# Kernel tuning notes

Hardware: AMD Instinct MI355X
Metric: run time of the kernel (lower is better)

Reference implementation:

```python
import jax, jax.numpy as jnp
import numpy as np
import math

NUM_REG_TOKENS = 0  # encoder.num_register_tokens
EPS = 1e-12         # matches torch F.normalize eps


def _l2norm(x):
    # F.normalize(x, dim=-1): x / max(||x||, eps)
    n = jnp.sqrt(jnp.sum(x * x, axis=-1, keepdims=True))
    return x / jnp.maximum(n, EPS)


def setup_inputs() -> dict:
    key = jax.random.key(0)
    k1, k2 = jax.random.split(key)
    L, N, S, T, D = 3, 8, 4, 1370, 768  # 3 interested layers, T = 1 + 37^2 patches
    q_feats = jax.random.normal(k1, (L, N, T, D), dtype=jnp.float32)
    s_feats = jax.random.normal(k2, (L, N * S, T, D), dtype=jnp.float32)
    return {"q_feats": q_feats, "s_feats": s_feats}


def reference(q_feats, s_feats):
    # fuse_feature: mean over stacked interested layers
    xq = jnp.mean(q_feats, axis=0)   # [N, T, D]
    xs = jnp.mean(s_feats, axis=0)   # [N*S, T, D]
    N = xq.shape[0]
    Q = xq.shape[1] - 1 - NUM_REG_TOKENS
    side = int(math.isqrt(Q))
    # drop class (+register) tokens
    xq = xq[:, 1 + NUM_REG_TOKENS:, :]                 # [N, Q, D]
    xs = xs[:, 1 + NUM_REG_TOKENS:, :]                 # [N*S, Q, D]
    xs = xs.reshape(N, -1, xs.shape[-1])               # [N, S*Q, D]
    xq = _l2norm(xq)
    xs = _l2norm(xs)
    # cosine distance + 1-NN min over support tokens
    sim = jnp.einsum('nqd,nsd->nqs', xq, xs)           # [N, Q, S*Q]
    dist = jnp.min(1.0 - sim, axis=-1)                 # [N, Q]
    return dist.reshape(N, 1, side, side)
```

## Files before the change

### kernel.cpp

```cpp
#include <hip/hip_runtime.h>
#include <hip/hip_bf16.h>

typedef __attribute__((ext_vector_type(4))) float f32x4;

#define T_TOK 1370
#define DDIM  768
#define SCV   1369
#define SCP   1408
#define MQP   1536
#define NB    8
#define NSLAB 32
#define NST   44
#define NMT   6

#define MEMFENCE asm volatile("" ::: "memory")
#define BARRIER  do { __builtin_amdgcn_s_barrier(); MEMFENCE; } while (0)

#define GLOAD_LDS16(g, l)                                                     \
  __builtin_amdgcn_global_load_lds(                                           \
      (const __attribute__((address_space(1))) unsigned int*)(g),             \
      (__attribute__((address_space(3))) unsigned int*)(l), 16, 0, 0)

extern "C" __global__ __launch_bounds__(192) void prep_kernel(
    const float* __restrict__ src, unsigned char* __restrict__ dst,
    size_t lstride)
{
  const int row  = blockIdx.x;
  const int slab = blockIdx.y;
  const int t    = threadIdx.x;
  unsigned char* drow = dst + ((size_t)slab * gridDim.x + row) * DDIM;
  if (row >= SCV) {
    reinterpret_cast<unsigned int*>(drow)[t] = 0u;
    return;
  }
  const float* base = src + ((size_t)slab * T_TOK + row + 1) * DDIM;
  float4 a = reinterpret_cast<const float4*>(base)[t];
  float4 b = reinterpret_cast<const float4*>(base + lstride)[t];
  float4 c = reinterpret_cast<const float4*>(base + 2 * lstride)[t];
  const float k3 = 1.0f / 3.0f;
  float4 m;
  m.x = (a.x + b.x + c.x) * k3;
  m.y = (a.y + b.y + c.y) * k3;
  m.z = (a.z + b.z + c.z) * k3;
  m.w = (a.w + b.w + c.w) * k3;
  float ss = m.x * m.x + m.y * m.y + m.z * m.z + m.w * m.w;
  #pragma unroll
  for (int d = 1; d < 64; d <<= 1) ss += __shfl_xor(ss, d);
  __shared__ float wsum[3];
  if ((t & 63) == 0) wsum[t >> 6] = ss;
  __syncthreads();
  float tot = wsum[0] + wsum[1] + wsum[2];
  float rn = 1.0f / fmaxf(sqrtf(tot), 1e-12f);
  int pk = __builtin_amdgcn_cvt_pk_fp8_f32(m.x * rn, m.y * rn, 0, false);
  pk = __builtin_amdgcn_cvt_pk_fp8_f32(m.z * rn, m.w * rn, pk, true);
  reinterpret_cast<unsigned int*>(drow)[t] = (unsigned int)pk;
}

extern "C" __global__ __launch_bounds__(256, 2) void simmax_kernel(
    const unsigned char* __restrict__ xq,
    const unsigned char* __restrict__ xs,
    float* __restrict__ part)
{
  const int flat = blockIdx.x + NMT * (blockIdx.y + NST * blockIdx.z);
  const int swz  = (flat & 7) * (NMT * NST) + (flat >> 3);
  const int mt   = swz % NMT;
  const int st   = (swz / NMT) % NST;
  const int n    = swz / (NMT * NST);

  const int tid = threadIdx.x;
  const int lane = tid & 63;
  const int w    = tid >> 6;
  const int wr = w >> 1;
  const int wc = w & 1;
  const int l15 = lane & 15, l4 = lane >> 4;

  __shared__ unsigned char ring[3][12288];

  const int slab = st / 11;
  const int lt   = st - slab * 11;
  const unsigned char* gA = xq + ((size_t)n * MQP + (size_t)mt * 256) * DDIM;
  const unsigned char* gB =
      xs + ((size_t)(n * 4 + slab) * SCP + (size_t)lt * 128) * DDIM;

  int aoffg[2], aldso[2], boffg0, bldso0;
  #pragma unroll
  for (int i = 0; i < 2; ++i) {
    int c = w * 2 + i;
    int r = c * 32 + (lane >> 1);
    aoffg[i] = r * DDIM + (((lane & 1) ^ ((r >> 2) & 1)) << 4);
    aldso[i] = c * 1024;
  }
  {
    int r = w * 32 + (lane >> 1);
    boffg0 = r * DDIM + (((lane & 1) ^ ((r >> 2) & 1)) << 4);
    bldso0 = 8192 + w * 1024;
  }

  const int kxor = (((l4 >> 1) ^ ((l15 >> 2) & 1)) << 4) + (l4 & 1) * 8;
  int aoff[8], boff[4];
  #pragma unroll
  for (int mf = 0; mf < 8; ++mf)
    aoff[mf] = (wr * 128 + mf * 16 + l15) * 32 + kxor;
  #pragma unroll
  for (int nf = 0; nf < 4; ++nf)
    boff[nf] = 8192 + (wc * 64 + nf * 16 + l15) * 32 + kxor;

  f32x4 acc[8][4];
  {
    f32x4 zz = {0.f, 0.f, 0.f, 0.f};
    #pragma unroll
    for (int a = 0; a < 8; ++a)
      #pragma unroll
      for (int b = 0; b < 4; ++b) acc[a][b] = zz;
  }

  #define ISSUE(KT, RB)                                                      \
    do {                                                                     \
      const unsigned char* ga_ = gA + (KT) * 32;                             \
      const unsigned char* gb_ = gB + (KT) * 32;                             \
      unsigned char* lb_ = ring[RB];                                         \
      _Pragma("unroll") for (int i = 0; i < 2; ++i)                          \
        GLOAD_LDS16(ga_ + aoffg[i], lb_ + aldso[i]);                         \
      GLOAD_LDS16(gb_ + boffg0, lb_ + bldso0);                               \
    } while (0)

  ISSUE(0, 0);
  ISSUE(1, 1);
  asm volatile("s_waitcnt vmcnt(3)" ::: "memory");
  BARRIER;

  for (int kt = 0; kt < 24; ++kt) {
    if (kt + 2 < 24) ISSUE(kt + 2, (kt + 2) % 3);

    const char* Cb = reinterpret_cast<const char*>(ring[kt % 3]);
    long bfr[4], af[8];
    #pragma unroll
    for (int nf = 0; nf < 4; ++nf)
      bfr[nf] = *reinterpret_cast<const long*>(Cb + boff[nf]);
    #pragma unroll
    for (int mf = 0; mf < 8; ++mf)
      af[mf] = *reinterpret_cast<const long*>(Cb + aoff[mf]);

    __builtin_amdgcn_s_setprio(1);
    #pragma unroll
    for (int mf = 0; mf < 8; ++mf)
      #pragma unroll
      for (int nf = 0; nf < 4; ++nf)
        acc[mf][nf] = __builtin_amdgcn_mfma_f32_16x16x32_fp8_fp8(
            af[mf], bfr[nf], acc[mf][nf], 0, 0, 0);
    __builtin_amdgcn_s_setprio(0);

    if (kt < 22)       asm volatile("s_waitcnt vmcnt(3)" ::: "memory");
    else if (kt == 22) asm volatile("s_waitcnt vmcnt(0)" ::: "memory");
    if (kt < 23) BARRIER;
  }

  float rmax[8][4];
  #pragma unroll
  for (int a = 0; a < 8; ++a)
    #pragma unroll
    for (int b = 0; b < 4; ++b) rmax[a][b] = -1e30f;

  #pragma unroll
  for (int nf = 0; nf < 4; ++nf) {
    int col = lt * 128 + wc * 64 + nf * 16 + l15;
    if (col < SCV) {
      #pragma unroll
      for (int mf = 0; mf < 8; ++mf)
        #pragma unroll
        for (int j = 0; j < 4; ++j)
          rmax[mf][j] = fmaxf(rmax[mf][j], acc[mf][nf][j]);
    }
  }

  #pragma unroll
  for (int msk = 1; msk < 16; msk <<= 1)
    #pragma unroll
    for (int mf = 0; mf < 8; ++mf)
      #pragma unroll
      for (int j = 0; j < 4; ++j)
        rmax[mf][j] = fmaxf(rmax[mf][j], __shfl_xor(rmax[mf][j], msk));

  __syncthreads();
  float* buf = reinterpret_cast<float*>(&ring[0][0]);
  if (l15 == 0) {
    #pragma unroll
    for (int mf = 0; mf < 8; ++mf)
      #pragma unroll
      for (int j = 0; j < 4; ++j) {
        int r = wr * 128 + mf * 16 + l4 * 4 + j;
        buf[wc * 256 + r] = rmax[mf][j];
      }
  }
  __syncthreads();
  if (tid < 256) {
    float v = fmaxf(buf[tid], buf[256 + tid]);
    part[((size_t)n * NST + st) * MQP + (size_t)mt * 256 + tid] = v;
  }
}

extern "C" __global__ void finalize_kernel(const float* __restrict__ part,
                                           float* __restrict__ out) {
  int i = blockIdx.x * 256 + threadIdx.x;
  if (i >= NB * SCV) return;
  int n = i / SCV, q = i - n * SCV;
  const float* p = part + (size_t)n * NST * MQP + q;
  float m = p[0];
  #pragma unroll 4
  for (int g = 1; g < NST; ++g) m = fmaxf(m, p[(size_t)g * MQP]);
  out[i] = 1.0f - m;
}

extern "C" void kernel_launch(void* const* d_in, const int* in_sizes, int n_in,
                              void* d_out, int out_size, void* d_ws, size_t ws_size,
                              hipStream_t stream) {
  const float* q_feats = (const float*)d_in[0];
  const float* s_feats = (const float*)d_in[1];
  float* out = (float*)d_out;

  char* ws = (char*)d_ws;
  const size_t xq_bytes = (size_t)NB * MQP * DDIM;
  const size_t xs_bytes = (size_t)NSLAB * SCP * DDIM;
  unsigned char* xq = (unsigned char*)ws;
  unsigned char* xs = (unsigned char*)(ws + xq_bytes);
  float* part       = (float*)(ws + xq_bytes + xs_bytes);

  prep_kernel<<<dim3(MQP, NB), 192, 0, stream>>>(
      q_feats, xq, (size_t)NB * T_TOK * DDIM);
  prep_kernel<<<dim3(SCP, NSLAB), 192, 0, stream>>>(
      s_feats, xs, (size_t)NSLAB * T_TOK * DDIM);
  simmax_kernel<<<dim3(NMT, NST, NB), 256, 0, stream>>>(xq, xs, part);
  finalize_kernel<<<dim3((NB * SCV + 255) / 256), 256, 0, stream>>>(part, out);
}
```

Baseline: 208.7 us.

## Use 16x16x128 scaled FP8 MFMA with larger 256x256 tiles and K=128 staging

Replaces the 16x16x32 FP8 MFMA with the gfx950 scaled 16x16x128 f8f6f4 MFMA, which does four times the K per instruction. Block tiles grow from 256x128 to 256x256 with 512 threads (8 waves). K is staged 128 bytes at a time into a double-buffered 128 KB LDS ring with an XOR swizzle. Support tiles now span slab boundaries, so padded-column masking uses modulo SCP, and the number of partial-max groups halves. The larger LDS footprint and thread count may reduce occupancy, and the shallower two-stage pipeline may expose load latency.

Measured after the change: 182.0 us (median of 2 runs). 12.8% less time.

```diff
diff --git a/kernel.cpp b/kernel.cpp
--- a/kernel.cpp
+++ b/kernel.cpp
@@ -2,6 +2,7 @@
 #include <hip/hip_bf16.h>
 
 typedef __attribute__((ext_vector_type(4))) float f32x4;
+typedef __attribute__((ext_vector_type(8))) int i32x8;
 
 #define T_TOK 1370
 #define DDIM  768
@@ -10,11 +11,12 @@
 #define MQP   1536
 #define NB    8
 #define NSLAB 32
-#define NST   44
+#define NST   22
 #define NMT   6
 
 #define MEMFENCE asm volatile("" ::: "memory")
 #define BARRIER  do { __builtin_amdgcn_s_barrier(); MEMFENCE; } while (0)
+#define VMCNT0   asm volatile("s_waitcnt vmcnt(0)" ::: "memory")
 
 #define GLOAD_LDS16(g, l)                                                     \
   __builtin_amdgcn_global_load_lds(                                           \
@@ -56,54 +58,51 @@
   reinterpret_cast<unsigned int*>(drow)[t] = (unsigned int)pk;
 }
 
-extern "C" __global__ __launch_bounds__(256, 2) void simmax_kernel(
+extern "C" __global__ __launch_bounds__(512, 2) void simmax_kernel(
     const unsigned char* __restrict__ xq,
     const unsigned char* __restrict__ xs,
     float* __restrict__ part)
 {
-  const int flat = blockIdx.x + NMT * (blockIdx.y + NST * blockIdx.z);
+  const int flat = blockIdx.x;
   const int swz  = (flat & 7) * (NMT * NST) + (flat >> 3);
-  const int mt   = swz % NMT;
-  const int st   = (swz / NMT) % NST;
   const int n    = swz / (NMT * NST);
-
-  const int tid = threadIdx.x;
+  const int idx  = swz - n * (NMT * NST);
+  const int mt   = idx % NMT;
+  const int st   = idx / NMT;
+
+  const int tid  = threadIdx.x;
   const int lane = tid & 63;
   const int w    = tid >> 6;
-  const int wr = w >> 1;
-  const int wc = w & 1;
-  const int l15 = lane & 15, l4 = lane >> 4;
-
-  __shared__ unsigned char ring[3][12288];
-
-  const int slab = st / 11;
-  const int lt   = st - slab * 11;
+  const int wr   = w >> 2;
+  const int wcn  = w & 3;
+  const int l15  = lane & 15, l4 = lane >> 4;
+
+  __shared__ unsigned char ring[2][65536];
+  __shared__ float sfold[1024];
+
   const unsigned char* gA = xq + ((size_t)n * MQP + (size_t)mt * 256) * DDIM;
-  const unsigned char* gB =
-      xs + ((size_t)(n * 4 + slab) * SCP + (size_t)lt * 128) * DDIM;
-
-  int aoffg[2], aldso[2], boffg0, bldso0;
-  #pragma unroll
-  for (int i = 0; i < 2; ++i) {
-    int c = w * 2 + i;
-    int r = c * 32 + (lane >> 1);
-    aoffg[i] = r * DDIM + (((lane & 1) ^ ((r >> 2) & 1)) << 4);
-    aldso[i] = c * 1024;
-  }
-  {
-    int r = w * 32 + (lane >> 1);
-    boffg0 = r * DDIM + (((lane & 1) ^ ((r >> 2) & 1)) << 4);
-    bldso0 = 8192 + w * 1024;
-  }
-
-  const int kxor = (((l4 >> 1) ^ ((l15 >> 2) & 1)) << 4) + (l4 & 1) * 8;
+  const unsigned char* gB = xs + ((size_t)n * 4 * SCP + (size_t)st * 256) * DDIM;
+
+  int goff[4], ldso[4];
+  #pragma unroll
+  for (int i = 0; i < 4; ++i) {
+    int c = w * 4 + i;
+    int r = c * 8 + (lane >> 3);
+    goff[i] = r * DDIM + (((lane & 7) ^ (r & 7)) << 4);
+    ldso[i] = c * 1024;
+  }
+
   int aoff[8], boff[4];
   #pragma unroll
-  for (int mf = 0; mf < 8; ++mf)
-    aoff[mf] = (wr * 128 + mf * 16 + l15) * 32 + kxor;
-  #pragma unroll
-  for (int nf = 0; nf < 4; ++nf)
-    boff[nf] = 8192 + (wc * 64 + nf * 16 + l15) * 32 + kxor;
+  for (int mf = 0; mf < 8; ++mf) {
+    int row = wr * 128 + mf * 16 + l15;
+    aoff[mf] = row * 128 + ((((l4 << 1) ^ (row & 7))) << 4);
+  }
+  #pragma unroll
+  for (int nf = 0; nf < 4; ++nf) {
+    int row = wcn * 64 + nf * 16 + l15;
+    boff[nf] = 32768 + row * 128 + ((((l4 << 1) ^ (row & 7))) << 4);
+  }
 
   f32x4 acc[8][4];
   {
@@ -116,85 +115,90 @@
 
   #define ISSUE(KT, RB)                                                      \
     do {                                                                     \
-      const unsigned char* ga_ = gA + (KT) * 32;                             \
-      const unsigned char* gb_ = gB + (KT) * 32;                             \
-      unsigned char* lb_ = ring[RB];                                         \
-      _Pragma("unroll") for (int i = 0; i < 2; ++i)                          \
-        GLOAD_LDS16(ga_ + aoffg[i], lb_ + aldso[i]);                         \
-      GLOAD_LDS16(gb_ + boffg0, lb_ + bldso0);                               \
+      const unsigned char* ga_ = gA + (KT) * 128;                            \
+      const unsigned char* gb_ = gB + (KT) * 128;                            \
+      unsigned char* la_ = ring[RB];                                         \
+      unsigned char* lb_ = ring[RB] + 32768;                                 \
+      _Pragma("unroll") for (int i = 0; i < 4; ++i)                          \
+        GLOAD_LDS16(ga_ + goff[i], la_ + ldso[i]);                           \
+      _Pragma("unroll") for (int i = 0; i < 4; ++i)                          \
+        GLOAD_LDS16(gb_ + goff[i], lb_ + ldso[i]);                           \
     } while (0)
 
   ISSUE(0, 0);
-  ISSUE(1, 1);
-  asm volatile("s_waitcnt vmcnt(3)" ::: "memory");
+  VMCNT0;
   BARRIER;
 
-  for (int kt = 0; kt < 24; ++kt) {
-    if (kt + 2 < 24) ISSUE(kt + 2, (kt + 2) % 3);
-
-    const char* Cb = reinterpret_cast<const char*>(ring[kt % 3]);
-    long bfr[4], af[8];
-    #pragma unroll
-    for (int nf = 0; nf < 4; ++nf)
-      bfr[nf] = *reinterpret_cast<const long*>(Cb + boff[nf]);
+  for (int kt = 0; kt < 6; ++kt) {
+    if (kt + 1 < 6) ISSUE(kt + 1, (kt + 1) & 1);
+
+    const char* Cb = reinterpret_cast<const char*>(ring[kt & 1]);
+    i32x8 bfr[4];
+    #pragma unroll
+    for (int nf = 0; nf < 4; ++nf) {
+      int4 lo = *reinterpret_cast<const int4*>(Cb + boff[nf]);
+      int4 hi = *reinterpret_cast<const int4*>(Cb + (boff[nf] ^ 16));
+      bfr[nf] = i32x8{lo.x, lo.y, lo.z, lo.w, hi.x, hi.y, hi.z, hi.w};
+    }
+    __builtin_amdgcn_s_setprio(1);
+    #pragma unroll
+    for (int mf = 0; mf < 8; ++mf) {
+      int4 lo = *reinterpret_cast<const int4*>(Cb + aoff[mf]);
+      int4 hi = *reinterpret_cast<const int4*>(Cb + (aoff[mf] ^ 16));
+      i32x8 af = i32x8{lo.x, lo.y, lo.z, lo.w, hi.x, hi.y, hi.z, hi.w};
+      #pragma unroll
+      for (int nf = 0; nf < 4; ++nf)
+        acc[mf][nf] = __builtin_amdgcn_mfma_scale_f32_16x16x128_f8f6f4(
+            af, bfr[nf], acc[mf][nf], 0, 0, 0, 127, 0, 127);
+    }
+    __builtin_amdgcn_s_setprio(0);
+
+    if (kt + 1 < 6) VMCNT0;
+    if (kt < 5) BARRIER;
+  }
+
+  bool colv[4];
+  #pragma unroll
+  for (int nf = 0; nf < 4; ++nf) {
+    int col = st * 256 + wcn * 64 + nf * 16 + l15;
+    int within = col - (col / SCP) * SCP;
+    colv[nf] = within < SCV;
+  }
+
+  float rm[8][4];
+  #pragma unroll
+  for (int mf = 0; mf < 8; ++mf)
+    #pragma unroll
+    for (int j = 0; j < 4; ++j) {
+      float v = -1e30f;
+      #pragma unroll
+      for (int nf = 0; nf < 4; ++nf)
+        if (colv[nf]) v = fmaxf(v, acc[mf][nf][j]);
+      rm[mf][j] = v;
+    }
+
+  #pragma unroll
+  for (int msk = 1; msk < 16; msk <<= 1)
     #pragma unroll
     for (int mf = 0; mf < 8; ++mf)
-      af[mf] = *reinterpret_cast<const long*>(Cb + aoff[mf]);
-
-    __builtin_amdgcn_s_setprio(1);
-    #pragma unroll
-    for (int mf = 0; mf < 8; ++mf)
-      #pragma unroll
-      for (int nf = 0; nf < 4; ++nf)
-        acc[mf][nf] = __builtin_amdgcn_mfma_f32_16x16x32_fp8_fp8(
-            af[mf], bfr[nf], acc[mf][nf], 0, 0, 0);
-    __builtin_amdgcn_s_setprio(0);
-
-    if (kt < 22)       asm volatile("s_waitcnt vmcnt(3)" ::: "memory");
-    else if (kt == 22) asm volatile("s_waitcnt vmcnt(0)" ::: "memory");
-    if (kt < 23) BARRIER;
-  }
-
-  float rmax[8][4];
-  #pragma unroll
-  for (int a = 0; a < 8; ++a)
-    #pragma unroll
-    for (int b = 0; b < 4; ++b) rmax[a][b] = -1e30f;
-
-  #pragma unroll
-  for (int nf = 0; nf < 4; ++nf) {
-    int col = lt * 128 + wc * 64 + nf * 16 + l15;
-    if (col < SCV) {
-      #pragma unroll
-      for (int mf = 0; mf < 8; ++mf)
-        #pragma unroll
-        for (int j = 0; j < 4; ++j)
-          rmax[mf][j] = fmaxf(rmax[mf][j], acc[mf][nf][j]);
-    }
-  }
-
-  #pragma unroll
-  for (int msk = 1; msk < 16; msk <<= 1)
-    #pragma unroll
-    for (int mf = 0; mf < 8; ++mf)
       #pragma unroll
       for (int j = 0; j < 4; ++j)
-        rmax[mf][j] = fmaxf(rmax[mf][j], __shfl_xor(rmax[mf][j], msk));
+        rm[mf][j] = fmaxf(rm[mf][j], __shfl_xor(rm[mf][j], msk));
 
   __syncthreads();
-  float* buf = reinterpret_cast<float*>(&ring[0][0]);
   if (l15 == 0) {
     #pragma unroll
     for (int mf = 0; mf < 8; ++mf)
       #pragma unroll
       for (int j = 0; j < 4; ++j) {
         int r = wr * 128 + mf * 16 + l4 * 4 + j;
-        buf[wc * 256 + r] = rmax[mf][j];
+        sfold[wcn * 256 + r] = rm[mf][j];
       }
   }
   __syncthreads();
   if (tid < 256) {
-    float v = fmaxf(buf[tid], buf[256 + tid]);
+    float v = fmaxf(fmaxf(sfold[tid], sfold[256 + tid]),
+                    fmaxf(sfold[512 + tid], sfold[768 + tid]));
     part[((size_t)n * NST + st) * MQP + (size_t)mt * 256 + tid] = v;
   }
 }
@@ -229,6 +233,6 @@
       q_feats, xq, (size_t)NB * T_TOK * DDIM);
   prep_kernel<<<dim3(SCP, NSLAB), 192, 0, stream>>>(
       s_feats, xs, (size_t)NSLAB * T_TOK * DDIM);
-  simmax_kernel<<<dim3(NMT, NST, NB), 256, 0, stream>>>(xq, xs, part);
+  simmax_kernel<<<dim3(NB * NMT * NST), 512, 0, stream>>>(xq, xs, part);
   finalize_kernel<<<dim3((NB * SCV + 255) / 256), 256, 0, stream>>>(part, out);
 }
```

## Switch FP8 GEMM to 32x32x64 scaled MFMA with 64-byte K tiles

Applied to the files above, without the earlier changes.

Replaces the 16x16x32 FP8 MFMA with the gfx950 32x32x64 f8f6f4 scaled MFMA (unit scales). The K tile per stage doubles to 64 bytes, which halves the number of pipeline iterations and barriers. The LDS ring buffer, the swizzled load layout and the row-max reduction over the 32x32 output layout are all reworked to match. This raises MFMA throughput per instruction and cuts sync overhead, at the cost of doubled LDS use per stage, which may affect occupancy.

After: 214.2 us. +2.6%, slower.

```diff
diff --git a/kernel.cpp b/kernel.cpp
--- a/kernel.cpp
+++ b/kernel.cpp
@@ -1,7 +1,8 @@
 #include <hip/hip_runtime.h>
 #include <hip/hip_bf16.h>
 
-typedef __attribute__((ext_vector_type(4))) float f32x4;
+typedef __attribute__((ext_vector_type(16))) float f32x16;
+typedef __attribute__((ext_vector_type(8))) int i32x8;
 
 #define T_TOK 1370
 #define DDIM  768
@@ -67,14 +68,15 @@
   const int st   = (swz / NMT) % NST;
   const int n    = swz / (NMT * NST);
 
-  const int tid = threadIdx.x;
+  const int tid  = threadIdx.x;
   const int lane = tid & 63;
   const int w    = tid >> 6;
-  const int wr = w >> 1;
-  const int wc = w & 1;
-  const int l15 = lane & 15, l4 = lane >> 4;
-
-  __shared__ unsigned char ring[3][12288];
+  const int wr   = w >> 1;
+  const int wc   = w & 1;
+  const int l31  = lane & 31;
+  const int h    = lane >> 5;
+
+  __shared__ unsigned char ring[3][24576];
 
   const int slab = st / 11;
   const int lt   = st - slab * 11;
@@ -82,114 +84,123 @@
   const unsigned char* gB =
       xs + ((size_t)(n * 4 + slab) * SCP + (size_t)lt * 128) * DDIM;
 
-  int aoffg[2], aldso[2], boffg0, bldso0;
+  int aoffg[4], aldso[4], boffg[2], bldso[2];
+  #pragma unroll
+  for (int i = 0; i < 4; ++i) {
+    int c = w * 4 + i;
+    int r = c * 16 + (lane >> 2);
+    aoffg[i] = r * DDIM + (((lane & 3) ^ (r & 3)) << 4);
+    aldso[i] = c * 1024;
+  }
   #pragma unroll
   for (int i = 0; i < 2; ++i) {
     int c = w * 2 + i;
-    int r = c * 32 + (lane >> 1);
-    aoffg[i] = r * DDIM + (((lane & 1) ^ ((r >> 2) & 1)) << 4);
-    aldso[i] = c * 1024;
-  }
+    int r = c * 16 + (lane >> 2);
+    boffg[i] = r * DDIM + (((lane & 3) ^ (r & 3)) << 4);
+    bldso[i] = 16384 + c * 1024;
+  }
+
+  int aoff[4], boff[2];
+  #pragma unroll
+  for (int mf = 0; mf < 4; ++mf) {
+    int row = wr * 128 + mf * 32 + l31;
+    aoff[mf] = row * 64 + ((((h << 1) ^ (row & 3))) << 4);
+  }
+  #pragma unroll
+  for (int nf = 0; nf < 2; ++nf) {
+    int row = wc * 64 + nf * 32 + l31;
+    boff[nf] = 16384 + row * 64 + ((((h << 1) ^ (row & 3))) << 4);
+  }
+
+  f32x16 acc[4][2];
   {
-    int r = w * 32 + (lane >> 1);
-    boffg0 = r * DDIM + (((lane & 1) ^ ((r >> 2) & 1)) << 4);
-    bldso0 = 8192 + w * 1024;
-  }
-
-  const int kxor = (((l4 >> 1) ^ ((l15 >> 2) & 1)) << 4) + (l4 & 1) * 8;
-  int aoff[8], boff[4];
-  #pragma unroll
-  for (int mf = 0; mf < 8; ++mf)
-    aoff[mf] = (wr * 128 + mf * 16 + l15) * 32 + kxor;
-  #pragma unroll
-  for (int nf = 0; nf < 4; ++nf)
-    boff[nf] = 8192 + (wc * 64 + nf * 16 + l15) * 32 + kxor;
-
-  f32x4 acc[8][4];
-  {
-    f32x4 zz = {0.f, 0.f, 0.f, 0.f};
-    #pragma unroll
-    for (int a = 0; a < 8; ++a)
-      #pragma unroll
-      for (int b = 0; b < 4; ++b) acc[a][b] = zz;
+    f32x16 zz = {0.f,0.f,0.f,0.f,0.f,0.f,0.f,0.f,
+                 0.f,0.f,0.f,0.f,0.f,0.f,0.f,0.f};
+    #pragma unroll
+    for (int a = 0; a < 4; ++a)
+      #pragma unroll
+      for (int b = 0; b < 2; ++b) acc[a][b] = zz;
   }
 
   #define ISSUE(KT, RB)                                                      \
     do {                                                                     \
-      const unsigned char* ga_ = gA + (KT) * 32;                             \
-      const unsigned char* gb_ = gB + (KT) * 32;                             \
+      const unsigned char* ga_ = gA + (KT) * 64;                             \
+      const unsigned char* gb_ = gB + (KT) * 64;                             \
       unsigned char* lb_ = ring[RB];                                         \
+      _Pragma("unroll") for (int i = 0; i < 4; ++i)                          \
+        GLOAD_LDS16(ga_ + aoffg[i], lb_ + aldso[i]);                         \
       _Pragma("unroll") for (int i = 0; i < 2; ++i)                          \
-        GLOAD_LDS16(ga_ + aoffg[i], lb_ + aldso[i]);                         \
-      GLOAD_LDS16(gb_ + boffg0, lb_ + bldso0);                               \
+        GLOAD_LDS16(gb_ + boffg[i], lb_ + bldso[i]);                         \
     } while (0)
 
   ISSUE(0, 0);
   ISSUE(1, 1);
-  asm volatile("s_waitcnt vmcnt(3)" ::: "memory");
+  asm volatile("s_waitcnt vmcnt(6)" ::: "memory");
   BARRIER;
 
-  for (int kt = 0; kt < 24; ++kt) {
-    if (kt + 2 < 24) ISSUE(kt + 2, (kt + 2) % 3);
+  for (int kt = 0; kt < 12; ++kt) {
+    if (kt + 2 < 12) ISSUE(kt + 2, (kt + 2) % 3);
 
     const char* Cb = reinterpret_cast<const char*>(ring[kt % 3]);
-    long bfr[4], af[8];
-    #pragma unroll
-    for (int nf = 0; nf < 4; ++nf)
-      bfr[nf] = *reinterpret_cast<const long*>(Cb + boff[nf]);
-    #pragma unroll
-    for (int mf = 0; mf < 8; ++mf)
-      af[mf] = *reinterpret_cast<const long*>(Cb + aoff[mf]);
-
+    i32x8 bfr[2];
+    #pragma unroll
+    for (int nf = 0; nf < 2; ++nf) {
+      int4 lo = *reinterpret_cast<const int4*>(Cb + boff[nf]);
+      int4 hi = *reinterpret_cast<const int4*>(Cb + (boff[nf] ^ 16));
+      bfr[nf] = i32x8{lo.x, lo.y, lo.z, lo.w, hi.x, hi.y, hi.z, hi.w};
+    }
     __builtin_amdgcn_s_setprio(1);
     #pragma unroll
-    for (int mf = 0; mf < 8; ++mf)
-      #pragma unroll
-      for (int nf = 0; nf < 4; ++nf)
-        acc[mf][nf] = __builtin_amdgcn_mfma_f32_16x16x32_fp8_fp8(
-            af[mf], bfr[nf], acc[mf][nf], 0, 0, 0);
+    for (int mf = 0; mf < 4; ++mf) {
+      int4 lo = *reinterpret_cast<const int4*>(Cb + aoff[mf]);
+      int4 hi = *reinterpret_cast<const int4*>(Cb + (aoff[mf] ^ 16));
+      i32x8 af = i32x8{lo.x, lo.y, lo.z, lo.w, hi.x, hi.y, hi.z, hi.w};
+      #pragma unroll
+      for (int nf = 0; nf < 2; ++nf)
+        acc[mf][nf] = __builtin_amdgcn_mfma_scale_f32_32x32x64_f8f6f4(
+            af, bfr[nf], acc[mf][nf], 0, 0, 0, 127, 0, 127);
+    }
     __builtin_amdgcn_s_setprio(0);
 
-    if (kt < 22)       asm volatile("s_waitcnt vmcnt(3)" ::: "memory");
-    else if (kt == 22) asm volatile("s_waitcnt vmcnt(0)" ::: "memory");
-    if (kt < 23) BARRIER;
-  }
-
-  float rmax[8][4];
-  #pragma unroll
-  for (int a = 0; a < 8; ++a)
-    #pragma unroll
-    for (int b = 0; b < 4; ++b) rmax[a][b] = -1e30f;
-
-  #pragma unroll
-  for (int nf = 0; nf < 4; ++nf) {
-    int col = lt * 128 + wc * 64 + nf * 16 + l15;
-    if (col < SCV) {
-      #pragma unroll
-      for (int mf = 0; mf < 8; ++mf)
-        #pragma unroll
-        for (int j = 0; j < 4; ++j)
-          rmax[mf][j] = fmaxf(rmax[mf][j], acc[mf][nf][j]);
+    if (kt < 10)       asm volatile("s_waitcnt vmcnt(6)" ::: "memory");
+    else if (kt == 10) asm volatile("s_waitcnt vmcnt(0)" ::: "memory");
+    if (kt < 11) BARRIER;
+  }
+
+  bool colv[2];
+  #pragma unroll
+  for (int nf = 0; nf < 2; ++nf)
+    colv[nf] = (lt * 128 + wc * 64 + nf * 32 + l31) < SCV;
+
+  float rm[4][16];
+  #pragma unroll
+  for (int mf = 0; mf < 4; ++mf)
+    #pragma unroll
+    for (int j = 0; j < 16; ++j) {
+      float v = -1e30f;
+      #pragma unroll
+      for (int nf = 0; nf < 2; ++nf)
+        if (colv[nf]) v = fmaxf(v, acc[mf][nf][j]);
+      rm[mf][j] = v;
     }
-  }
-
-  #pragma unroll
-  for (int msk = 1; msk < 16; msk <<= 1)
-    #pragma unroll
-    for (int mf = 0; mf < 8; ++mf)
-      #pragma unroll
-      for (int j = 0; j < 4; ++j)
-        rmax[mf][j] = fmaxf(rmax[mf][j], __shfl_xor(rmax[mf][j], msk));
+
+  #pragma unroll
+  for (int msk = 1; msk < 32; msk <<= 1)
+    #pragma unroll
+    for (int mf = 0; mf < 4; ++mf)
+      #pragma unroll
+      for (int j = 0; j < 16; ++j)
+        rm[mf][j] = fmaxf(rm[mf][j], __shfl_xor(rm[mf][j], msk));
 
   __syncthreads();
   float* buf = reinterpret_cast<float*>(&ring[0][0]);
-  if (l15 == 0) {
-    #pragma unroll
-    for (int mf = 0; mf < 8; ++mf)
-      #pragma unroll
-      for (int j = 0; j < 4; ++j) {
-        int r = wr * 128 + mf * 16 + l4 * 4 + j;
-        buf[wc * 256 + r] = rmax[mf][j];
+  if (l31 == 0) {
+    #pragma unroll
+    for (int mf = 0; mf < 4; ++mf)
+      #pragma unroll
+      for (int j = 0; j < 16; ++j) {
+        int r = wr * 128 + mf * 32 + (j & 3) + 8 * (j >> 2) + 4 * h;
+        buf[wc * 256 + r] = rm[mf][j];
       }
   }
   __syncthreads();
```
